# Performance work log

Hardware: AMD Instinct MI355X
Metric: run time of the kernel (lower is better)

Reference implementation:

```python
import jax, jax.numpy as jnp
import numpy as np
import math

N_BLOBS = 20
DT = 0.01
TWO_PI = 2.0 * math.pi


def pos_enc(x, L=4):
    # torch: for f in 2**linspace(0,L-1,L): append sin(2*pi*f*x), cos(2*pi*f*x)
    freqs = [2.0 ** i for i in range(L)]
    return jnp.concatenate(
        [fn(TWO_PI * f * x) for f in freqs for fn in (jnp.sin, jnp.cos)], axis=-1
    )  # (N, 3*2*L)


def dynamics(state, dyn_w1, dyn_b1, dyn_w2, dyn_b2, coupling, damping, interaction):
    # state: (n_blobs, 8) = [pos(3), vel(3), size(1), intensity(1)]
    flat = state.reshape(-1)  # (160,)
    h = jnp.tanh(dyn_w1 @ flat + dyn_b1)
    dneural = (dyn_w2 @ h + dyn_b2).reshape(N_BLOBS, 8)
    pos = state[:, :3]
    vel = state[:, 3:6]
    sizes = state[:, 6:7]
    intens = state[:, 7:8]
    diffs = pos[:, None, :] - pos[None, :, :]          # (B,B,3)
    dists = jnp.sqrt(jnp.sum(diffs ** 2, axis=-1) + 1e-6)  # (B,B)
    force_mag = interaction / (dists ** 2 + 1.0)
    force_dir = diffs / (dists[:, :, None] + 1e-6)
    forces = jnp.sum(force_mag[:, :, None] * force_dir, axis=1)  # (B,3)
    dvel = -damping * vel + coupling * forces + dneural[:, 3:6]
    dsize = -0.05 * (sizes - 1.0) + dneural[:, 6:7]
    dintens = -0.05 * (intens - 0.5) + dneural[:, 7:8]
    return jnp.concatenate([vel, dvel, dsize, dintens], axis=-1)


def setup_inputs() -> dict:
    key = jax.random.key(0)
    ks = jax.random.split(key, 16)
    N = 2097152
    inp = {
        "p": jax.random.normal(ks[0], (N, 3), dtype=jnp.float32),
        "initial_state": jax.random.normal(ks[1], (N_BLOBS, 8), dtype=jnp.float32) * 0.3,
        "dyn_w1": jax.random.uniform(ks[2], (64, 160), jnp.float32, -1, 1) / np.sqrt(160),
        "dyn_b1": jax.random.uniform(ks[3], (64,), jnp.float32, -1, 1) / np.sqrt(160),
        "dyn_w2": jax.random.uniform(ks[4], (160, 64), jnp.float32, -1, 1) / np.sqrt(64),
        "dyn_b2": jax.random.uniform(ks[5], (160,), jnp.float32, -1, 1) / np.sqrt(64),
        "coupling": jnp.ones((1,), jnp.float32) * 0.5,
        "damping": jnp.ones((1,), jnp.float32) * 0.1,
        "interaction": jax.random.normal(ks[6], (N_BLOBS, N_BLOBS), dtype=jnp.float32) * 0.1,
        "summ_w": jax.random.uniform(ks[7], (32, 160), jnp.float32, -1, 1) / np.sqrt(160),
        "summ_b": jax.random.uniform(ks[8], (32,), jnp.float32, -1, 1) / np.sqrt(160),
        "fq_w1": jax.random.uniform(ks[9], (64, 56), jnp.float32, -1, 1) / np.sqrt(56),
        "fq_b1": jax.random.uniform(ks[10], (64,), jnp.float32, -1, 1) / np.sqrt(56),
        "fq_w2": jax.random.uniform(ks[11], (1, 64), jnp.float32, -1, 1) / np.sqrt(64),
        "fq_b2": jax.random.uniform(ks[12], (1,), jnp.float32, -1, 1) / np.sqrt(64),
        "col_w1": jax.random.uniform(ks[13], (64, 57), jnp.float32, -1, 1) / np.sqrt(57),
        "col_b1": jax.random.uniform(ks[14], (64,), jnp.float32, -1, 1) / np.sqrt(57),
        "col_w2": jax.random.uniform(ks[15], (3, 64), jnp.float32, -1, 1) / np.sqrt(64),
        "col_b2": jnp.zeros((3,), jnp.float32),
        "t": 2,
    }
    return inp


def reference(p, initial_state, dyn_w1, dyn_b1, dyn_w2, dyn_b2, coupling, damping,
              interaction, summ_w, summ_b, fq_w1, fq_b1, fq_w2, fq_b2,
              col_w1, col_b1, col_w2, col_b2, t):
    # --- evolve_state: Euler ODE integration (n_steps sequential steps) ---
    n_steps = max(1, int(t / DT))
    actual_dt = jnp.float32(t / n_steps)

    def step(state, _):
        ds = dynamics(state, dyn_w1, dyn_b1, dyn_w2, dyn_b2, coupling, damping, interaction)
        return state + actual_dt * ds, None

    blob_state, _ = jax.lax.scan(step, initial_state, None, length=n_steps)

    # --- query_field ---
    p_enc = pos_enc(p, L=4)                              # (N, 24)
    summary = summ_w @ blob_state.reshape(-1) + summ_b   # (32,)
    summary_exp = jnp.broadcast_to(summary[None, :], (p.shape[0], summary.shape[0]))
    field_in = jnp.concatenate([p_enc, summary_exp], axis=-1)  # (N, 56)
    h = jax.nn.relu(field_in @ fq_w1.T + fq_b1)
    density = jax.nn.softplus(h @ fq_w2.T + fq_b2)       # (N, 1)
    color_in = jnp.concatenate([p_enc, summary_exp, density], axis=-1)  # (N, 57)
    hc = jax.nn.relu(color_in @ col_w1.T + col_b1)
    color = jax.nn.sigmoid(hc @ col_w2.T + col_b2)       # (N, 3)
    return density, color
```

## Files before the change

### kernel.cpp

```cpp
#include <hip/hip_runtime.h>
#include <math.h>

#define NB 20
#define SDIM 160
#define H1 64
#define TWO_PI_F 6.28318530717958647692f

#define WS_DFRAG 0
#define WS_CFRAG 2048
#define WS_DBEFF 4096
#define WS_DW2   4160
#define WS_CBEFF 4224
#define WS_WD    4288
#define WS_W2C0  4352
#define WS_W2C1  4416
#define WS_W2C2  4480
#define WS_MISC2 4544
#define WS_FLAG  4552
#define FLAG_MAGIC0 0x13579BDF
#define FLAG_MAGIC1 0x2468ACE1

typedef short  bf16x8 __attribute__((ext_vector_type(8)));
typedef float  f32x4  __attribute__((ext_vector_type(4)));

__device__ __forceinline__ float fast_sigmoid(float x){ return 1.0f/(1.0f+__expf(-x)); }
__device__ __forceinline__ float fast_softplus(float x){
    return fmaxf(x, 0.0f) + __logf(1.0f + __expf(-fabsf(x)));
}
__device__ __forceinline__ float fast_rcp(float x){ return __builtin_amdgcn_rcpf(x); }
__device__ __forceinline__ float fast_rsq(float x){ return __builtin_amdgcn_rsqf(x); }
__device__ __forceinline__ float bperm(float v, int srcLane){
    return __int_as_float(__builtin_amdgcn_ds_bpermute(srcLane << 2, __float_as_int(v)));
}
__device__ __forceinline__ float rdlane(float v, int l){
    return __int_as_float(__builtin_amdgcn_readlane(__float_as_int(v), l));
}
__device__ __forceinline__ float getS(float s0, float s1, float s2, int f){
    return (f < 64) ? rdlane(s0, f) : (f < 128) ? rdlane(s1, f - 64) : rdlane(s2, f - 128);
}
__device__ __forceinline__ unsigned short bf16rn(float f){
    unsigned int u = __float_as_uint(f);
    unsigned int r = u + 0x7FFFu + ((u >> 16) & 1u);
    return (unsigned short)(r >> 16);
}
__device__ __forceinline__ float bf16tof(unsigned short h){
    return __uint_as_float(((unsigned int)h) << 16);
}
__device__ __forceinline__ f32x4 mfma_bf16(uint4 a, uint4 b, f32x4 c){
    return __builtin_amdgcn_mfma_f32_16x16x32_bf16(
        __builtin_bit_cast(bf16x8, a), __builtin_bit_cast(bf16x8, b), c, 0, 0, 0);
}

__global__ __launch_bounds__(256) void fused_kernel(
    const float* __restrict__ p,
    const float* __restrict__ initial_state,
    const float* __restrict__ dyn_w1, const float* __restrict__ dyn_b1,
    const float* __restrict__ dyn_w2, const float* __restrict__ dyn_b2,
    const float* __restrict__ couplingP, const float* __restrict__ dampingP,
    const float* __restrict__ interaction,
    const float* __restrict__ summ_w, const float* __restrict__ summ_b,
    const float* __restrict__ fq_w1, const float* __restrict__ fq_b1,
    const float* __restrict__ fq_w2, const float* __restrict__ fq_b2,
    const float* __restrict__ col_w1, const float* __restrict__ col_b1,
    const float* __restrict__ col_w2, const float* __restrict__ col_b2,
    const int* __restrict__ tP,
    float* ws, float* out, int N)
{
    __shared__ float sP1L[3*64];
    __shared__ float sDnP[4*128];
    __shared__ float sFr[64];
    __shared__ float sPosL[64];
    __shared__ float sSum[32];
    __shared__ unsigned int arena[4*2560];

    const int tid  = threadIdx.x;
    const int w    = tid >> 6;
    const int lane = tid & 63;

    if (blockIdx.x == 0){
        const int wv = w;

        if (tid < 60) sPosL[tid] = initial_state[(tid/3)*8 + (tid - (tid/3)*3)];
        __syncthreads();

        float w1s[54];
        if (wv < 3){
            const int kb = wv*53;
            #pragma unroll
            for (int t2 = 0; t2 < 54; ++t2) w1s[t2] = dyn_w1[lane*SDIM + kb + t2];
        }
        float w2a16[16], w2b16[16];
        {
            const int kb2 = wv*16;
            const int rowA = (lane/5)*8 + 3 + (lane - (lane/5)*5);
            const int o2   = 64 + lane;
            const int rowB = (o2 < 100) ? (o2/5)*8 + 3 + (o2 - (o2/5)*5) : 0;
            const bool vb  = (o2 < 100);
            #pragma unroll
            for (int t2 = 0; t2 < 16; ++t2){
                w2a16[t2] = dyn_w2[rowA*H1 + kb2 + t2];
                w2b16[t2] = vb ? dyn_w2[rowB*H1 + kb2 + t2] : 0.0f;
            }
        }

        const int fi  = lane % 20;
        const int jg  = lane / 20;
        const int jj0 = jg * 7;
        float rintw[7];
        #pragma unroll
        for (int u = 0; u < 7; ++u){
            int jj = jj0 + u;
            rintw[u] = (wv == 3 && lane < 60 && jj < NB) ? interaction[fi*NB + jj] : 0.0f;
        }

        float s0 = initial_state[lane];
        float s1 = initial_state[64 + lane];
        float s2 = (lane < 32) ? initial_state[128 + lane] : 0.0f;

        const float b1r = dyn_b1[lane];
        float b2ar, b2br;
        { int b = lane/5, c = lane - (lane/5)*5; b2ar = dyn_b2[b*8 + 3 + c]; }
        { int o2 = 64 + lane;
          if (o2 < 100){ int b = o2/5, c = o2 - (o2/5)*5; b2br = dyn_b2[b*8 + 3 + c]; }
          else b2br = 0.0f; }
        const float bA0 = (wv == 0) ? b2ar : 0.0f;
        const float bB0 = (wv == 0) ? b2br : 0.0f;

        const float coupling = couplingP[0];
        const float damping  = dampingP[0];
        const int tv = tP[0];
        int n_steps = (int)((double)tv / 0.01);
        if (n_steps < 1) n_steps = 1;
        const float adt = (float)((double)tv / (double)n_steps);

        const int cc  = lane & 7;
        const int bb  = lane >> 3;
        const int cm3 = (cc >= 3) ? cc - 3 : 0;
        const int lp3 = (lane + 3 > 63) ? 63 : lane + 3;

        for (int step = 0; step < n_steps; ++step){
            float fx = 0.f, fy = 0.f, fz = 0.f;
            if (wv < 3){
                float aa[4] = {0.f, 0.f, 0.f, 0.f};
                if (wv == 0){
                    #pragma unroll
                    for (int t2 = 0; t2 < 53; ++t2)
                        aa[t2&3] = fmaf(rdlane(s0, t2), w1s[t2], aa[t2&3]);
                } else if (wv == 1){
                    #pragma unroll
                    for (int t2 = 0; t2 < 53; ++t2){
                        int k = 53 + t2;
                        float sv = (k < 64) ? rdlane(s0, k) : rdlane(s1, k - 64);
                        aa[t2&3] = fmaf(sv, w1s[t2], aa[t2&3]);
                    }
                } else {
                    #pragma unroll
                    for (int t2 = 0; t2 < 54; ++t2){
                        int k = 106 + t2;
                        float sv = (k < 128) ? rdlane(s1, k - 64) : rdlane(s2, k - 128);
                        aa[t2&3] = fmaf(sv, w1s[t2], aa[t2&3]);
                    }
                }
                sP1L[wv*64 + lane] = (aa[0] + aa[1]) + (aa[2] + aa[3]);
            } else {
                float px = sPosL[fi*3+0], py = sPosL[fi*3+1], pz = sPosL[fi*3+2];
                #pragma unroll
                for (int u = 0; u < 7; ++u){
                    int jj = jj0 + u;
                    int js = (jj < NB) ? jj : 0;
                    float dx = px - sPosL[js*3+0];
                    float dy = py - sPosL[js*3+1];
                    float dz = pz - sPosL[js*3+2];
                    float e  = fmaf(dx,dx, fmaf(dy,dy, fmaf(dz,dz, 1e-6f)));
                    float d  = e * fast_rsq(e);
                    float mag = rintw[u] * fast_rcp(e + 1.0f);
                    float w_  = mag * fast_rcp(d + 1e-6f);
                    fx = fmaf(dx, w_, fx);
                    fy = fmaf(dy, w_, fy);
                    fz = fmaf(dz, w_, fz);
                }
                fx += bperm(fx, lane+20) + bperm(fx, lane+40);
                fy += bperm(fy, lane+20) + bperm(fy, lane+40);
                fz += bperm(fz, lane+20) + bperm(fz, lane+40);
            }

            __syncthreads();

            if (wv == 3 && lane < NB){
                sFr[lane*3+0] = fx; sFr[lane*3+1] = fy; sFr[lane*3+2] = fz;
            }

            float hv = (sP1L[lane] + sP1L[64 + lane]) + sP1L[128 + lane] + b1r;
            hv = fminf(fmaxf(hv, -15.0f), 15.0f);
            float e2v = __expf(2.0f * hv);
            float hreg = (e2v - 1.0f) * fast_rcp(e2v + 1.0f);

            {
                float dA0=0.f, dA1=0.f, dB0=0.f, dB1=0.f;
                const int kb2 = wv*16;
                #pragma unroll
                for (int t2 = 0; t2 < 16; t2 += 2){
                    float h0 = rdlane(hreg, kb2 + t2);
                    float h1 = rdlane(hreg, kb2 + t2 + 1);
                    dA0 = fmaf(h0, w2a16[t2],   dA0);
                    dA1 = fmaf(h1, w2a16[t2+1], dA1);
                    dB0 = fmaf(h0, w2b16[t2],   dB0);
                    dB1 = fmaf(h1, w2b16[t2+1], dB1);
                }
                sDnP[wv*128 + lane]      = dA0 + dA1 + bA0;
                sDnP[wv*128 + 64 + lane] = dB0 + dB1 + bB0;
            }

            __syncthreads();

            {
                float v0 = bperm(s0, lp3);
                float v1 = bperm(s1, lp3);
                float v2 = bperm(s2, lp3);
                int o0 = bb*5 + cm3;
                int o1 = 40 + o0;
                int o2 = 80 + o0;
                float dn0 = (sDnP[o0] + sDnP[128 + o0]) + (sDnP[256 + o0] + sDnP[384 + o0]);
                float dn1 = (sDnP[o1] + sDnP[128 + o1]) + (sDnP[256 + o1] + sDnP[384 + o1]);
                float dn2 = (sDnP[o2] + sDnP[128 + o2]) + (sDnP[256 + o2] + sDnP[384 + o2]);
                float F0 = sFr[bb*3 + cm3];
                float F1 = sFr[(8+bb)*3 + cm3];
                float F2 = sFr[(lane < 32) ? (16+bb)*3 + cm3 : 0];

                float dv0 = (cc < 3) ? v0
                          : (cc < 6) ? fmaf(-damping, s0, fmaf(coupling, F0, dn0))
                          : (cc == 6) ? fmaf(-0.05f, s0 - 1.0f, dn0)
                                      : fmaf(-0.05f, s0 - 0.5f, dn0);
                float dv1 = (cc < 3) ? v1
                          : (cc < 6) ? fmaf(-damping, s1, fmaf(coupling, F1, dn1))
                          : (cc == 6) ? fmaf(-0.05f, s1 - 1.0f, dn1)
                                      : fmaf(-0.05f, s1 - 0.5f, dn1);
                float dv2 = (cc < 3) ? v2
                          : (cc < 6) ? fmaf(-damping, s2, fmaf(coupling, F2, dn2))
                          : (cc == 6) ? fmaf(-0.05f, s2 - 1.0f, dn2)
                                      : fmaf(-0.05f, s2 - 0.5f, dn2);

                s0 = fmaf(adt, dv0, s0);
                s1 = fmaf(adt, dv1, s1);
                s2 = fmaf(adt, dv2, s2);

                if (wv == 3 && cc < 3){
                    sPosL[bb*3 + cc]      = s0;
                    sPosL[(8+bb)*3 + cc]  = s1;
                    if (lane < 32) sPosL[(16+bb)*3 + cc] = s2;
                }
            }
        }

        if (wv == 0){
            {
                int sbase = (lane & 31) * SDIM;
                float sa = summ_b[lane & 31];
                #pragma unroll
                for (int k = 0; k < SDIM; ++k)
                    sa = fmaf(getS(s0,s1,s2,k), summ_w[sbase + k], sa);
                if (lane < 32) sSum[lane] = sa;
            }
            {
                float bq = fq_b1[lane], bc = col_b1[lane];
                #pragma unroll
                for (int m = 0; m < 32; ++m){
                    bq = fmaf(sSum[m], fq_w1[lane*56 + 24 + m], bq);
                    bc = fmaf(sSum[m], col_w1[lane*57 + 24 + m], bc);
                }
                ws[WS_DBEFF + lane] = bq;
                ws[WS_DW2   + lane] = fq_w2[lane];
                ws[WS_CBEFF + lane] = bc;
                ws[WS_WD    + lane] = col_w1[lane*57 + 56];
                ws[WS_W2C0  + lane] = col_w2[lane];
                ws[WS_W2C1  + lane] = col_w2[64 + lane];
                ws[WS_W2C2  + lane] = col_w2[128 + lane];
            }
            if (lane == 0){
                ws[WS_MISC2 + 0] = fq_b2[0];
                ws[WS_MISC2 + 1] = col_b2[0];
                ws[WS_MISC2 + 2] = col_b2[1];
                ws[WS_MISC2 + 3] = col_b2[2];
            }
            {
                unsigned int* wsu = (unsigned int*)ws;
                const int colc = lane & 15;
                const int kg   = lane >> 4;
                #pragma unroll
                for (int u = 0; u < 4; ++u){
                    const int n = u*16 + colc;
                    unsigned int hd[4], ldv[4], hc[4], lc[4];
                    #pragma unroll
                    for (int d = 0; d < 4; ++d){
                        unsigned short hh[2], hl[2], ch[2], cl[2];
                        #pragma unroll
                        for (int e = 0; e < 2; ++e){
                            const int k = kg*8 + d*2 + e;
                            float wd_ = (k < 24) ? fq_w1[n*56 + k]  : 0.0f;
                            float wc_ = (k < 24) ? col_w1[n*57 + k] : 0.0f;
                            hh[e] = bf16rn(wd_); hl[e] = bf16rn(wd_ - bf16tof(hh[e]));
                            ch[e] = bf16rn(wc_); cl[e] = bf16rn(wc_ - bf16tof(ch[e]));
                        }
                        hd[d]  = (unsigned int)hh[0] | ((unsigned int)hh[1] << 16);
                        ldv[d] = (unsigned int)hl[0] | ((unsigned int)hl[1] << 16);
                        hc[d]  = (unsigned int)ch[0] | ((unsigned int)ch[1] << 16);
                        lc[d]  = (unsigned int)cl[0] | ((unsigned int)cl[1] << 16);
                    }
                    *(uint4*)(wsu + WS_DFRAG + ((u*2+0)*64 + lane)*4) = make_uint4(hd[0],hd[1],hd[2],hd[3]);
                    *(uint4*)(wsu + WS_DFRAG + ((u*2+1)*64 + lane)*4) = make_uint4(ldv[0],ldv[1],ldv[2],ldv[3]);
                    *(uint4*)(wsu + WS_CFRAG + ((u*2+0)*64 + lane)*4) = make_uint4(hc[0],hc[1],hc[2],hc[3]);
                    *(uint4*)(wsu + WS_CFRAG + ((u*2+1)*64 + lane)*4) = make_uint4(lc[0],lc[1],lc[2],lc[3]);
                }
            }
        }
        __syncthreads();
        __threadfence();
        if (tid == 0){
            __hip_atomic_store((int*)(ws + WS_FLAG) + 1, FLAG_MAGIC1,
                               __ATOMIC_RELEASE, __HIP_MEMORY_SCOPE_AGENT);
            __hip_atomic_store((int*)(ws + WS_FLAG) + 0, FLAG_MAGIC0,
                               __ATOMIC_RELEASE, __HIP_MEMORY_SCOPE_AGENT);
        }
        return;
    }

    {
        const int* flagp = (const int*)(ws + WS_FLAG);
        if (tid == 0){
            for (;;){
                int f0 = __hip_atomic_load(flagp + 0, __ATOMIC_ACQUIRE, __HIP_MEMORY_SCOPE_AGENT);
                int f1 = __hip_atomic_load(flagp + 1, __ATOMIC_ACQUIRE, __HIP_MEMORY_SCOPE_AGENT);
                if (f0 == FLAG_MAGIC0 && f1 == FLAG_MAGIC1) break;
                __builtin_amdgcn_s_sleep(64);
            }
        }
        __syncthreads();
        (void)__hip_atomic_load((const int*)(ws + WS_FLAG), __ATOMIC_ACQUIRE, __HIP_MEMORY_SCOPE_AGENT);
    }

    unsigned int* AhW = &arena[w*2560];
    unsigned int* AlW = &arena[w*2560 + 1280];
    float* red  = (float*)&arena[w*2560];
    float* dpts = (float*)&arena[w*2560 + 1088];

    const unsigned int* wsu = (const unsigned int*)ws;
    const int ncol = lane & 15;
    const int kg   = lane >> 4;
    const int arow = lane & 15;
    const int aoff = kg * 4;
    const float m0  = ws[WS_MISC2 + 0];
    const float mc0 = ws[WS_MISC2 + 1];
    const float mc1 = ws[WS_MISC2 + 2];
    const float mc2 = ws[WS_MISC2 + 3];
    float* oc = out + N;

    const int nCons = (int)gridDim.x - 1;
    for (int b0 = ((int)blockIdx.x - 1) * 256; b0 < N; b0 += nCons * 256){
        const int base = b0 + w * 64;
        int i = base + lane; if (i >= N) i = N - 1;

        float t24[24];
        {
            const float a0 = p[3*i], a1 = p[3*i+1], a2 = p[3*i+2];
            #pragma unroll
            for (int f = 0; f < 4; ++f){
                const float wf = TWO_PI_F * (float)(1 << f);
                float s, c;
                __sincosf(wf * a0, &s, &c); t24[f*6+0]=s; t24[f*6+3]=c;
                __sincosf(wf * a1, &s, &c); t24[f*6+1]=s; t24[f*6+4]=c;
                __sincosf(wf * a2, &s, &c); t24[f*6+2]=s; t24[f*6+5]=c;
            }
        }
        unsigned int hiR[16], loR[16];
        #pragma unroll
        for (int q = 0; q < 12; ++q){
            unsigned short h0 = bf16rn(t24[2*q]);
            unsigned short h1 = bf16rn(t24[2*q+1]);
            unsigned short l0 = bf16rn(t24[2*q]   - bf16tof(h0));
            unsigned short l1 = bf16rn(t24[2*q+1] - bf16tof(h1));
            hiR[q] = (unsigned int)h0 | ((unsigned int)h1 << 16);
            loR[q] = (unsigned int)l0 | ((unsigned int)l1 << 16);
        }
        #pragma unroll
        for (int q = 12; q < 16; ++q){ hiR[q] = 0u; loR[q] = 0u; }

        #pragma unroll
        for (int d = 0; d < 4; ++d){
            *(uint4*)(AhW + lane*20 + d*4) = make_uint4(hiR[d*4],hiR[d*4+1],hiR[d*4+2],hiR[d*4+3]);
            *(uint4*)(AlW + lane*20 + d*4) = make_uint4(loR[d*4],loR[d*4+1],loR[d*4+2],loR[d*4+3]);
        }

        uint4 Ah[4], Al[4];
        #pragma unroll
        for (int t = 0; t < 4; ++t){
            Ah[t] = *(const uint4*)(AhW + (t*16 + arow)*20 + aoff);
            Al[t] = *(const uint4*)(AlW + (t*16 + arow)*20 + aoff);
        }

        float sd[4][4];
        #pragma unroll
        for (int t = 0; t < 4; ++t){ sd[t][0]=0.f; sd[t][1]=0.f; sd[t][2]=0.f; sd[t][3]=0.f; }
        #pragma unroll
        for (int u = 0; u < 4; ++u){
            uint4 Bh = *(const uint4*)(wsu + WS_DFRAG + ((u*2+0)*64 + lane)*4);
            uint4 Bl = *(const uint4*)(wsu + WS_DFRAG + ((u*2+1)*64 + lane)*4);
            float beff = ws[WS_DBEFF + u*16 + ncol];
            float w2   = ws[WS_DW2   + u*16 + ncol];
            #pragma unroll
            for (int t = 0; t < 4; ++t){
                f32x4 acc = {0.f,0.f,0.f,0.f};
                acc = mfma_bf16(Ah[t], Bh, acc);
                acc = mfma_bf16(Ah[t], Bl, acc);
                acc = mfma_bf16(Al[t], Bh, acc);
                #pragma unroll
                for (int r = 0; r < 4; ++r){
                    float v = fmaxf(acc[r] + beff, 0.0f);
                    sd[t][r] = fmaf(v, w2, sd[t][r]);
                }
            }
        }
        #pragma unroll
        for (int t = 0; t < 4; ++t)
        #pragma unroll
        for (int r = 0; r < 4; ++r)
            red[(t*16 + kg*4 + r)*17 + ncol] = sd[t][r];
        float dsum = 0.f;
        #pragma unroll
        for (int c = 0; c < 16; ++c) dsum += red[lane*17 + c];
        const float densOwn = fast_softplus(dsum + m0);
        dpts[lane] = densOwn;

        float dens[4][4];
        #pragma unroll
        for (int t = 0; t < 4; ++t)
        #pragma unroll
        for (int r = 0; r < 4; ++r)
            dens[t][r] = dpts[t*16 + kg*4 + r];

        float c0s[4][4], c1s[4][4], c2s[4][4];
        #pragma unroll
        for (int t = 0; t < 4; ++t)
        #pragma unroll
        for (int r = 0; r < 4; ++r){ c0s[t][r]=0.f; c1s[t][r]=0.f; c2s[t][r]=0.f; }
        #pragma unroll
        for (int u = 0; u < 4; ++u){
            uint4 Bh = *(const uint4*)(wsu + WS_CFRAG + ((u*2+0)*64 + lane)*4);
            uint4 Bl = *(const uint4*)(wsu + WS_CFRAG + ((u*2+1)*64 + lane)*4);
            float beff = ws[WS_CBEFF + u*16 + ncol];
            float wd   = ws[WS_WD    + u*16 + ncol];
            float w2a  = ws[WS_W2C0  + u*16 + ncol];
            float w2b  = ws[WS_W2C1  + u*16 + ncol];
            float w2c  = ws[WS_W2C2  + u*16 + ncol];
            #pragma unroll
            for (int t = 0; t < 4; ++t){
                f32x4 acc = {0.f,0.f,0.f,0.f};
                acc = mfma_bf16(Ah[t], Bh, acc);
                acc = mfma_bf16(Ah[t], Bl, acc);
                acc = mfma_bf16(Al[t], Bh, acc);
                #pragma unroll
                for (int r = 0; r < 4; ++r){
                    float a = fmaf(dens[t][r], wd, acc[r] + beff);
                    a = fmaxf(a, 0.0f);
                    c0s[t][r] = fmaf(a, w2a, c0s[t][r]);
                    c1s[t][r] = fmaf(a, w2b, c1s[t][r]);
                    c2s[t][r] = fmaf(a, w2c, c2s[t][r]);
                }
            }
        }
        float cOwn[3];
        #pragma unroll
        for (int ch = 0; ch < 3; ++ch){
            #pragma unroll
            for (int t = 0; t < 4; ++t)
            #pragma unroll
            for (int r = 0; r < 4; ++r){
                float v = (ch == 0) ? c0s[t][r] : (ch == 1) ? c1s[t][r] : c2s[t][r];
                red[(t*16 + kg*4 + r)*17 + ncol] = v;
            }
            float s = 0.f;
            #pragma unroll
            for (int c = 0; c < 16; ++c) s += red[lane*17 + c];
            cOwn[ch] = s;
        }

        const int idx = base + lane;
        if (idx < N){
            out[idx] = densOwn;
            oc[3*idx + 0] = fast_sigmoid(cOwn[0] + mc0);
            oc[3*idx + 1] = fast_sigmoid(cOwn[1] + mc1);
            oc[3*idx + 2] = fast_sigmoid(cOwn[2] + mc2);
        }
    }
}

extern "C" void kernel_launch(void* const* d_in, const int* in_sizes, int n_in,
                              void* d_out, int out_size, void* d_ws, size_t ws_size,
                              hipStream_t stream)
{
    const float* p             = (const float*)d_in[0];
    const float* initial_state = (const float*)d_in[1];
    const float* dyn_w1        = (const float*)d_in[2];
    const float* dyn_b1        = (const float*)d_in[3];
    const float* dyn_w2        = (const float*)d_in[4];
    const float* dyn_b2        = (const float*)d_in[5];
    const float* coupling      = (const float*)d_in[6];
    const float* damping       = (const float*)d_in[7];
    const float* interaction   = (const float*)d_in[8];
    const float* summ_w        = (const float*)d_in[9];
    const float* summ_b        = (const float*)d_in[10];
    const float* fq_w1         = (const float*)d_in[11];
    const float* fq_b1         = (const float*)d_in[12];
    const float* fq_w2         = (const float*)d_in[13];
    const float* fq_b2         = (const float*)d_in[14];
    const float* col_w1        = (const float*)d_in[15];
    const float* col_b1        = (const float*)d_in[16];
    const float* col_w2        = (const float*)d_in[17];
    const float* col_b2        = (const float*)d_in[18];
    const int*   tP            = (const int*)d_in[19];

    float* ws  = (float*)d_ws;
    float* out = (float*)d_out;
    const int N = in_sizes[0] / 3;

    int blocksPerCU = 0;
    (void)hipOccupancyMaxActiveBlocksPerMultiprocessor(&blocksPerCU,
            (const void*)fused_kernel, 256, 0);
    if (blocksPerCU < 1) blocksPerCU = 1;
    int numCU = 0;
    (void)hipDeviceGetAttribute(&numCU, hipDeviceAttributeMultiprocessorCount, 0);
    if (numCU < 1) numCU = 256;
    long long grid = (long long)blocksPerCU * numCU;
    if (grid < 2) grid = 2;
    if (grid > 4096) grid = 4096;

    hipLaunchKernelGGL(fused_kernel, dim3((unsigned)grid), dim3(256), 0, stream,
                       p, initial_state, dyn_w1, dyn_b1, dyn_w2, dyn_b2,
                       coupling, damping, interaction, summ_w, summ_b,
                       fq_w1, fq_b1, fq_w2, fq_b2,
                       col_w1, col_b1, col_w2, col_b2, tP,
                       ws, out, N);
}
```

Measured before the change: 229.1 us.

## Remove one barrier per ODE step via redundant layer-2 and double-buffered LDS

```diff
diff --git a/kernel.cpp b/kernel.cpp
--- a/kernel.cpp
+++ b/kernel.cpp
@@ -66,9 +66,8 @@
     const int* __restrict__ tP,
     float* ws, float* out, int N)
 {
-    __shared__ float sP1L[3*64];
-    __shared__ float sDnP[4*128];
-    __shared__ float sFr[64];
+    __shared__ float sP1L[2*192];
+    __shared__ float sFrD[2*64];
     __shared__ float sPosL[64];
     __shared__ float sSum[32];
     __shared__ unsigned int arena[4*2560];
@@ -89,17 +88,16 @@
             #pragma unroll
             for (int t2 = 0; t2 < 54; ++t2) w1s[t2] = dyn_w1[lane*SDIM + kb + t2];
         }
-        float w2a16[16], w2b16[16];
+        float w2a[64], w2b[64];
         {
-            const int kb2 = wv*16;
             const int rowA = (lane/5)*8 + 3 + (lane - (lane/5)*5);
             const int o2   = 64 + lane;
             const int rowB = (o2 < 100) ? (o2/5)*8 + 3 + (o2 - (o2/5)*5) : 0;
             const bool vb  = (o2 < 100);
             #pragma unroll
-            for (int t2 = 0; t2 < 16; ++t2){
-                w2a16[t2] = dyn_w2[rowA*H1 + kb2 + t2];
-                w2b16[t2] = vb ? dyn_w2[rowB*H1 + kb2 + t2] : 0.0f;
+            for (int k = 0; k < 64; ++k){
+                w2a[k] = dyn_w2[rowA*H1 + k];
+                w2b[k] = vb ? dyn_w2[rowB*H1 + k] : 0.0f;
             }
         }
 
@@ -123,8 +121,6 @@
         { int o2 = 64 + lane;
           if (o2 < 100){ int b = o2/5, c = o2 - (o2/5)*5; b2br = dyn_b2[b*8 + 3 + c]; }
           else b2br = 0.0f; }
-        const float bA0 = (wv == 0) ? b2ar : 0.0f;
-        const float bB0 = (wv == 0) ? b2br : 0.0f;
 
         const float coupling = couplingP[0];
         const float damping  = dampingP[0];
@@ -138,8 +134,8 @@
         const int cm3 = (cc >= 3) ? cc - 3 : 0;
         const int lp3 = (lane + 3 > 63) ? 63 : lane + 3;
 
+        int par = 0;
         for (int step = 0; step < n_steps; ++step){
-            float fx = 0.f, fy = 0.f, fz = 0.f;
             if (wv < 3){
                 float aa[4] = {0.f, 0.f, 0.f, 0.f};
                 if (wv == 0){
@@ -161,9 +157,10 @@
                         aa[t2&3] = fmaf(sv, w1s[t2], aa[t2&3]);
                     }
                 }
-                sP1L[wv*64 + lane] = (aa[0] + aa[1]) + (aa[2] + aa[3]);
+                sP1L[par*192 + wv*64 + lane] = (aa[0] + aa[1]) + (aa[2] + aa[3]);
             } else {
                 float px = sPosL[fi*3+0], py = sPosL[fi*3+1], pz = sPosL[fi*3+2];
+                float fx = 0.f, fy = 0.f, fz = 0.f;
                 #pragma unroll
                 for (int u = 0; u < 7; ++u){
                     int jj = jj0 + u;
@@ -182,36 +179,32 @@
                 fx += bperm(fx, lane+20) + bperm(fx, lane+40);
                 fy += bperm(fy, lane+20) + bperm(fy, lane+40);
                 fz += bperm(fz, lane+20) + bperm(fz, lane+40);
+                if (lane < NB){
+                    sFrD[par*64 + lane*3+0] = fx;
+                    sFrD[par*64 + lane*3+1] = fy;
+                    sFrD[par*64 + lane*3+2] = fz;
+                }
             }
 
             __syncthreads();
 
-            if (wv == 3 && lane < NB){
-                sFr[lane*3+0] = fx; sFr[lane*3+1] = fy; sFr[lane*3+2] = fz;
-            }
-
-            float hv = (sP1L[lane] + sP1L[64 + lane]) + sP1L[128 + lane] + b1r;
+            float hv = (sP1L[par*192 + lane] + sP1L[par*192 + 64 + lane])
+                     + sP1L[par*192 + 128 + lane] + b1r;
             hv = fminf(fmaxf(hv, -15.0f), 15.0f);
             float e2v = __expf(2.0f * hv);
             float hreg = (e2v - 1.0f) * fast_rcp(e2v + 1.0f);
 
-            {
-                float dA0=0.f, dA1=0.f, dB0=0.f, dB1=0.f;
-                const int kb2 = wv*16;
-                #pragma unroll
-                for (int t2 = 0; t2 < 16; t2 += 2){
-                    float h0 = rdlane(hreg, kb2 + t2);
-                    float h1 = rdlane(hreg, kb2 + t2 + 1);
-                    dA0 = fmaf(h0, w2a16[t2],   dA0);
-                    dA1 = fmaf(h1, w2a16[t2+1], dA1);
-                    dB0 = fmaf(h0, w2b16[t2],   dB0);
-                    dB1 = fmaf(h1, w2b16[t2+1], dB1);
-                }
-                sDnP[wv*128 + lane]      = dA0 + dA1 + bA0;
-                sDnP[wv*128 + 64 + lane] = dB0 + dB1 + bB0;
-            }
-
-            __syncthreads();
+            float dA0=0.f, dA1=0.f, dB0=0.f, dB1=0.f;
+            #pragma unroll
+            for (int k = 0; k < 64; k += 2){
+                float h0 = rdlane(hreg, k), h1 = rdlane(hreg, k+1);
+                dA0 = fmaf(h0, w2a[k],   dA0);
+                dA1 = fmaf(h1, w2a[k+1], dA1);
+                dB0 = fmaf(h0, w2b[k],   dB0);
+                dB1 = fmaf(h1, w2b[k+1], dB1);
+            }
+            float dnA = dA0 + dA1 + b2ar;
+            float dnB = dB0 + dB1 + b2br;
 
             {
                 float v0 = bperm(s0, lp3);
@@ -220,12 +213,14 @@
                 int o0 = bb*5 + cm3;
                 int o1 = 40 + o0;
                 int o2 = 80 + o0;
-                float dn0 = (sDnP[o0] + sDnP[128 + o0]) + (sDnP[256 + o0] + sDnP[384 + o0]);
-                float dn1 = (sDnP[o1] + sDnP[128 + o1]) + (sDnP[256 + o1] + sDnP[384 + o1]);
-                float dn2 = (sDnP[o2] + sDnP[128 + o2]) + (sDnP[256 + o2] + sDnP[384 + o2]);
-                float F0 = sFr[bb*3 + cm3];
-                float F1 = sFr[(8+bb)*3 + cm3];
-                float F2 = sFr[(lane < 32) ? (16+bb)*3 + cm3 : 0];
+                float dn0  = bperm(dnA, o0);
+                float dn1a = bperm(dnA, (o1 < 64) ? o1 : 0);
+                float dn1b = bperm(dnB, (o1 >= 64) ? o1 - 64 : 0);
+                float dn1  = (o1 < 64) ? dn1a : dn1b;
+                float dn2  = bperm(dnB, (o2 - 64) & 63);
+                float F0 = sFrD[par*64 + bb*3 + cm3];
+                float F1 = sFrD[par*64 + (8+bb)*3 + cm3];
+                float F2 = sFrD[par*64 + ((lane < 32) ? (16+bb)*3 + cm3 : 0)];
 
                 float dv0 = (cc < 3) ? v0
                           : (cc < 6) ? fmaf(-damping, s0, fmaf(coupling, F0, dn0))
@@ -250,6 +245,7 @@
                     if (lane < 32) sPosL[(16+bb)*3 + cc] = s2;
                 }
             }
+            par ^= 1;
         }
 
         if (wv == 0){
@@ -448,9 +444,9 @@
             uint4 Bl = *(const uint4*)(wsu + WS_CFRAG + ((u*2+1)*64 + lane)*4);
             float beff = ws[WS_CBEFF + u*16 + ncol];
             float wd   = ws[WS_WD    + u*16 + ncol];
-            float w2a  = ws[WS_W2C0  + u*16 + ncol];
-            float w2b  = ws[WS_W2C1  + u*16 + ncol];
-            float w2c  = ws[WS_W2C2  + u*16 + ncol];
+            float w2a_ = ws[WS_W2C0  + u*16 + ncol];
+            float w2b_ = ws[WS_W2C1  + u*16 + ncol];
+            float w2c_ = ws[WS_W2C2  + u*16 + ncol];
             #pragma unroll
             for (int t = 0; t < 4; ++t){
                 f32x4 acc = {0.f,0.f,0.f,0.f};
@@ -461,9 +457,9 @@
                 for (int r = 0; r < 4; ++r){
                     float a = fmaf(dens[t][r], wd, acc[r] + beff);
                     a = fmaxf(a, 0.0f);
-                    c0s[t][r] = fmaf(a, w2a, c0s[t][r]);
-                    c1s[t][r] = fmaf(a, w2b, c1s[t][r]);
-                    c2s[t][r] = fmaf(a, w2c, c2s[t][r]);
+                    c0s[t][r] = fmaf(a, w2a_, c0s[t][r]);
+                    c1s[t][r] = fmaf(a, w2b_, c1s[t][r]);
+                    c2s[t][r] = fmaf(a, w2c_, c2s[t][r]);
                 }
             }
         }
```

After: 319.7 us. 1.4x slower.
